# Optimization experiments

Measured on AMD Instinct MI355X. Metric: run time of the kernel, lower is better.

## Reference

```python
import jax, jax.numpy as jnp
import numpy as np

NV, NC, E, D = 100000, 400000, 1600000, 128

def _mlp2(x, w1, b1, w2, b2):
    # Linear->ReLU->Linear->ReLU (weights stored [in, out])
    return jax.nn.relu(jax.nn.relu(x @ w1 + b1) @ w2 + b2)

def setup_inputs() -> dict:
    key = jax.random.key(0)
    ks = jax.random.split(key, 16)
    s = 1.0 / np.sqrt(D)
    return {
        "hv": jax.random.normal(ks[0], (NV, D), jnp.float32),
        "hc": jax.random.normal(ks[1], (NC, D), jnp.float32),
        "row_v": jax.random.randint(ks[2], (E,), 0, NV, jnp.int32),
        "col_v": jax.random.randint(ks[3], (E,), 0, 2 * NC, jnp.int32),
        "row_c": jax.random.randint(ks[4], (E,), 0, NC, jnp.int32),
        "col_c": jax.random.randint(ks[5], (E,), 0, 2 * NV, jnp.int32),
        # message MLPs: order [fmv_pos, fmv_neg, fmc_pos, fmc_neg]
        "mw1": jax.random.normal(ks[6], (4, D, D), jnp.float32) * s,
        "mb1": jax.random.normal(ks[7], (4, D), jnp.float32) * s,
        "mw2": jax.random.normal(ks[8], (4, D, D), jnp.float32) * s,
        "mb2": jax.random.normal(ks[9], (4, D), jnp.float32) * s,
        # update MLPs: order [fuv, fuc]; first layer takes concat(h, m) -> 2D in
        "uw1": jax.random.normal(ks[10], (2, 2 * D, D), jnp.float32) * s,
        "ub1": jax.random.normal(ks[11], (2, D), jnp.float32) * s,
        "uw2": jax.random.normal(ks[12], (2, D, D), jnp.float32) * s,
        "ub2": jax.random.normal(ks[13], (2, D), jnp.float32) * s,
    }

def reference(hv, hc, row_v, col_v, row_c, col_c,
              mw1, mb1, mw2, mb2, uw1, ub1, uw2, ub2):
    nv, nc = hv.shape[0], hc.shape[0]
    # message: transform clause feats with pos/neg MLPs, concat rows, spmm via gather+segment_sum
    zv = jnp.concatenate([
        _mlp2(hc, mw1[0], mb1[0], mw2[0], mb2[0]),  # fmv_pos(hc)
        _mlp2(hc, mw1[1], mb1[1], mw2[1], mb2[1]),  # fmv_neg(hc)
    ], axis=0)                                       # [2*NC, D]
    mv = jax.ops.segment_sum(zv[col_v], row_v, num_segments=nv)  # spmm(vadj, zv)
    zc = jnp.concatenate([
        _mlp2(hv, mw1[2], mb1[2], mw2[2], mb2[2]),  # fmc_pos(hv)
        _mlp2(hv, mw1[3], mb1[3], mw2[3], mb2[3]),  # fmc_neg(hv)
    ], axis=0)                                       # [2*NV, D]
    mc = jax.ops.segment_sum(zc[col_c], row_c, num_segments=nc)  # spmm(cadj, zc)
    # update: concat(h, m) -> MLP
    hv_new = _mlp2(jnp.concatenate([hv, mv], axis=1), uw1[0], ub1[0], uw2[0], ub2[0])
    hc_new = _mlp2(jnp.concatenate([hc, mc], axis=1), uw1[1], ub1[1], uw2[1], ub2[1])
    return (hv_new, hc_new)
```

## Files before the change

kernel.cpp:

```cpp
#include <hip/hip_runtime.h>
#include <hip/hip_bf16.h>

#define NVV 100000
#define NCC 400000
#define NEE 1600000

typedef short short8 __attribute__((ext_vector_type(8)));
typedef short short4v __attribute__((ext_vector_type(4)));
typedef float f32x4 __attribute__((ext_vector_type(4)));
typedef unsigned int u32x2 __attribute__((ext_vector_type(2)));
typedef unsigned int u32x4 __attribute__((ext_vector_type(4)));

__device__ __forceinline__ float b2f(short s) {
    unsigned int u = ((unsigned int)(unsigned short)s) << 16;
    return __builtin_bit_cast(float, u);
}
__device__ __forceinline__ short f2b(float f) {
    __hip_bfloat16 h = __float2bfloat16(f);
    return __builtin_bit_cast(short, h);
}
__device__ __forceinline__ unsigned int cvtpk(float a, float b) {
    unsigned int r;
    asm("v_cvt_pk_bf16_f32 %0, %1, %2" : "=v"(r) : "v"(a), "v"(b));
    return r;
}

__global__ __launch_bounds__(256)
void prep_all(const float* __restrict__ mw1, const float* __restrict__ mw2,
              const float* __restrict__ uw1, const float* __restrict__ uw2,
              short* __restrict__ wt_m1, short* __restrict__ wt_m2,
              short* __restrict__ wt_u1, short* __restrict__ wt_u2)
{
    int e = blockIdx.x * 256 + threadIdx.x;
    const float* W; short* WT; int K; int idx;
    if (e < 65536)        { W = mw1; WT = wt_m1; K = 128; idx = e; }
    else if (e < 131072)  { W = mw2; WT = wt_m2; K = 128; idx = e - 65536; }
    else if (e < 196608)  { W = uw1; WT = wt_u1; K = 256; idx = e - 131072; }
    else if (e < 229376)  { W = uw2; WT = wt_u2; K = 128; idx = e - 196608; }
    else return;
    int mk = idx >> 7, n = idx & 127;
    int mi = mk / K, k = mk - mi * K;
    WT[(size_t)mi * K * 128 + (size_t)n * K + k] = f2b(W[idx]);
}

__global__ __launch_bounds__(256)
void to_bf16_2(const float* __restrict__ hv, const float* __restrict__ hc,
               short* __restrict__ hvb, short* __restrict__ hcb)
{
    const long nv = (long)NVV * 128;
    const long nc = (long)NCC * 128;
    long i0 = ((long)blockIdx.x * 256 + threadIdx.x) * 8;
    long stride = (long)gridDim.x * 256 * 8;
    for (long i = i0; i < nv + nc; i += stride) {
        const float* in; short* outp; long j;
        if (i < nv) { in = hv; outp = hvb; j = i; }
        else        { in = hc; outp = hcb; j = i - nv; }
        f32x4 a = *(const f32x4*)(in + j);
        f32x4 b = *(const f32x4*)(in + j + 4);
        u32x4 o;
        o[0] = cvtpk(a[0], a[1]);
        o[1] = cvtpk(a[2], a[3]);
        o[2] = cvtpk(b[0], b[1]);
        o[3] = cvtpk(b[2], b[3]);
        *(u32x4*)(outp + j) = o;
    }
}

template<int NW>
__global__ __launch_bounds__(NW * 64, 1)
void mlp2_msg_all(const short* __restrict__ hcb, const short* __restrict__ hvb,
                  const short* __restrict__ WT1, const float* __restrict__ B1a,
                  const short* __restrict__ WT2, const float* __restrict__ B2a,
                  short* __restrict__ zv, short* __restrict__ zc, int splitC)
{
    constexpr int BM = NW * 32;
    constexpr int NT = NW * 64;
    __shared__ short sW1[128 * 136];
    __shared__ short sW2[128 * 136];
    __shared__ short sH[BM * 136];

    const int tid = threadIdx.x;
    const int lane = tid & 63;
    const int w = tid >> 6;
    const int p = lane & 15;
    const int q = lane >> 4;

    int b = blockIdx.x;
    const short* X; short* z; int M, c0, cstr, set;
    if (b < splitC) {
        set = b & 1; X = hcb; z = zv + (size_t)set * NCC * 128;
        M = NCC; c0 = b >> 1; cstr = splitC >> 1;
    } else {
        int bb = b - splitC;
        set = 2 + (bb & 1); X = hvb; z = zc + (size_t)(bb & 1) * NVV * 128;
        M = NVV; c0 = bb >> 1; cstr = (gridDim.x - splitC) >> 1;
    }
    const int nChunks = (M + BM - 1) / BM;

    const short* w1g = WT1 + set * 16384;
    const short* w2g = WT2 + set * 16384;
    const float* b1g = B1a + set * 128;
    const float* b2g = B2a + set * 128;

    for (int e = tid * 8; e < 128 * 128; e += NT * 8) {
        int n = e >> 7, k = e & 127;
        *(short8*)(sW1 + n * 136 + k) = *(const short8*)(w1g + e);
        *(short8*)(sW2 + n * 136 + k) = *(const short8*)(w2g + e);
    }
    __syncthreads();

    if (c0 >= nChunks) return;

    short8 xfA[2][4], xfB[2][4];

    auto issueX = [&](short8 (&xf)[2][4], int c) {
        long base = (long)c * BM + w * 32;
        #pragma unroll
        for (int t = 0; t < 2; ++t) {
            long m = base + t * 16 + p;
            if (m > (long)M - 1) m = (long)M - 1;
            const short* src = X + m * 128 + q * 8;
            #pragma unroll
            for (int kk = 0; kk < 4; ++kk)
                xf[t][kk] = *(const short8*)(src + kk * 32);
        }
        __builtin_amdgcn_sched_barrier(0);
    };

    auto computeStore = [&](short8 (&xf)[2][4], int c) {
        long base = (long)c * BM + w * 32;
        f32x4 acc[8][2];
        #pragma unroll
        for (int cc = 0; cc < 8; ++cc)
            #pragma unroll
            for (int t = 0; t < 2; ++t)
                acc[cc][t] = (f32x4){0.f, 0.f, 0.f, 0.f};

        #pragma unroll
        for (int kk = 0; kk < 4; ++kk) {
            short8 af[8];
            #pragma unroll
            for (int cc = 0; cc < 8; ++cc)
                af[cc] = *(const short8*)(sW1 + (cc * 16 + p) * 136 + kk * 32 + q * 8);
            #pragma unroll
            for (int cc = 0; cc < 8; ++cc)
                #pragma unroll
                for (int t = 0; t < 2; ++t)
                    acc[cc][t] = __builtin_amdgcn_mfma_f32_16x16x32_bf16(af[cc], xf[t][kk], acc[cc][t], 0, 0, 0);
        }

        #pragma unroll
        for (int cc = 0; cc < 8; ++cc) {
            f32x4 bb = *(const f32x4*)(b1g + cc * 16 + q * 4);
            #pragma unroll
            for (int t = 0; t < 2; ++t) {
                u32x2 u;
                u[0] = cvtpk(fmaxf(acc[cc][t][0] + bb[0], 0.f), fmaxf(acc[cc][t][1] + bb[1], 0.f));
                u[1] = cvtpk(fmaxf(acc[cc][t][2] + bb[2], 0.f), fmaxf(acc[cc][t][3] + bb[3], 0.f));
                *(u32x2*)(sH + (w * 32 + t * 16 + p) * 136 + cc * 16 + q * 4) = u;
            }
        }
        asm volatile("s_waitcnt lgkmcnt(0)" ::: "memory");

        f32x4 acc2[8][2];
        #pragma unroll
        for (int cc = 0; cc < 8; ++cc)
            #pragma unroll
            for (int t = 0; t < 2; ++t)
                acc2[cc][t] = (f32x4){0.f, 0.f, 0.f, 0.f};

        #pragma unroll
        for (int kk = 0; kk < 4; ++kk) {
            short8 af[8], bfr[2];
            #pragma unroll
            for (int cc = 0; cc < 8; ++cc)
                af[cc] = *(const short8*)(sW2 + (cc * 16 + p) * 136 + kk * 32 + q * 8);
            #pragma unroll
            for (int t = 0; t < 2; ++t)
                bfr[t] = *(const short8*)(sH + (w * 32 + t * 16 + p) * 136 + kk * 32 + q * 8);
            #pragma unroll
            for (int cc = 0; cc < 8; ++cc)
                #pragma unroll
                for (int t = 0; t < 2; ++t)
                    acc2[cc][t] = __builtin_amdgcn_mfma_f32_16x16x32_bf16(af[cc], bfr[t], acc2[cc][t], 0, 0, 0);
        }

        #pragma unroll
        for (int cc = 0; cc < 8; ++cc) {
            f32x4 bb = *(const f32x4*)(b2g + cc * 16 + q * 4);
            #pragma unroll
            for (int t = 0; t < 2; ++t) {
                long m = base + t * 16 + p;
                if (m < M) {
                    u32x2 u;
                    u[0] = cvtpk(fmaxf(acc2[cc][t][0] + bb[0], 0.f), fmaxf(acc2[cc][t][1] + bb[1], 0.f));
                    u[1] = cvtpk(fmaxf(acc2[cc][t][2] + bb[2], 0.f), fmaxf(acc2[cc][t][3] + bb[3], 0.f));
                    *(u32x2*)(z + m * 128 + cc * 16 + q * 4) = u;
                }
            }
        }
    };

    int c = c0;
    issueX(xfA, c);
    while (true) {
        if (c + cstr < nChunks) issueX(xfB, c + cstr);
        computeStore(xfA, c);
        c += cstr; if (c >= nChunks) break;
        if (c + cstr < nChunks) issueX(xfA, c + cstr);
        computeStore(xfB, c);
        c += cstr; if (c >= nChunks) break;
    }
}

template<int NW>
__global__ __launch_bounds__(NW * 64, 1)
void mlp2_upd_all(const short* __restrict__ hvb, const short* __restrict__ hcb,
                  const short* __restrict__ mv, const short* __restrict__ mc,
                  const short* __restrict__ wt_u1, const float* __restrict__ ub1,
                  const short* __restrict__ wt_u2, const float* __restrict__ ub2,
                  float* __restrict__ out, int splitV)
{
    constexpr int BM = NW * 32;
    constexpr int NT = NW * 64;
    __shared__ short sW1[128 * 264];
    __shared__ short sW2[128 * 136];
    __shared__ short sH[BM * 136];

    const int tid = threadIdx.x;
    const int lane = tid & 63;
    const int w = tid >> 6;
    const int p = lane & 15;
    const int q = lane >> 4;

    int b = blockIdx.x;
    const short *X, *X2; float* O; int M, c0, cstr, set;
    if (b < splitV) {
        set = 0; X = hvb; X2 = mv; O = out; M = NVV; c0 = b; cstr = splitV;
    } else {
        set = 1; X = hcb; X2 = mc; O = out + (size_t)NVV * 128; M = NCC;
        c0 = b - splitV; cstr = gridDim.x - splitV;
    }
    const int nChunks = (M + BM - 1) / BM;

    const short* W1T = wt_u1 + set * 32768;
    const short* W2T = wt_u2 + set * 16384;
    const float* B1 = ub1 + set * 128;
    const float* B2 = ub2 + set * 128;

    for (int e = tid * 8; e < 128 * 256; e += NT * 8) {
        int n = e >> 8, k = e & 255;
        *(short8*)(sW1 + n * 264 + k) = *(const short8*)(W1T + e);
    }
    for (int e = tid * 8; e < 128 * 128; e += NT * 8) {
        int n = e >> 7, k = e & 127;
        *(short8*)(sW2 + n * 136 + k) = *(const short8*)(W2T + e);
    }
    __syncthreads();

    if (c0 >= nChunks) return;

    short8 bufA[2][8], bufB[2][8];

    auto issueX = [&](short8 (&xf)[2][8], int c) {
        long base = (long)c * BM + w * 32;
        #pragma unroll
        for (int t = 0; t < 2; ++t) {
            long m = base + t * 16 + p;
            if (m > (long)M - 1) m = (long)M - 1;
            const short* s1 = X + m * 128 + q * 8;
            const short* s2 = X2 + m * 128 + q * 8;
            #pragma unroll
            for (int kk = 0; kk < 4; ++kk) {
                xf[t][kk]     = *(const short8*)(s1 + kk * 32);
                xf[t][kk + 4] = *(const short8*)(s2 + kk * 32);
            }
        }
        __builtin_amdgcn_sched_barrier(0);
    };

    auto computeStore = [&](short8 (&xf)[2][8], int c) {
        long base = (long)c * BM + w * 32;
        f32x4 acc[8][2];
        #pragma unroll
        for (int cc = 0; cc < 8; ++cc)
            #pragma unroll
            for (int t = 0; t < 2; ++t)
                acc[cc][t] = (f32x4){0.f, 0.f, 0.f, 0.f};

        #pragma unroll
        for (int kk = 0; kk < 8; ++kk) {
            short8 af[8];
            #pragma unroll
            for (int cc = 0; cc < 8; ++cc)
                af[cc] = *(const short8*)(sW1 + (cc * 16 + p) * 264 + kk * 32 + q * 8);
            #pragma unroll
            for (int cc = 0; cc < 8; ++cc)
                #pragma unroll
                for (int t = 0; t < 2; ++t)
                    acc[cc][t] = __builtin_amdgcn_mfma_f32_16x16x32_bf16(af[cc], xf[t][kk], acc[cc][t], 0, 0, 0);
        }

        #pragma unroll
        for (int cc = 0; cc < 8; ++cc) {
            f32x4 bb = *(const f32x4*)(B1 + cc * 16 + q * 4);
            #pragma unroll
            for (int t = 0; t < 2; ++t) {
                u32x2 u;
                u[0] = cvtpk(fmaxf(acc[cc][t][0] + bb[0], 0.f), fmaxf(acc[cc][t][1] + bb[1], 0.f));
                u[1] = cvtpk(fmaxf(acc[cc][t][2] + bb[2], 0.f), fmaxf(acc[cc][t][3] + bb[3], 0.f));
                *(u32x2*)(sH + (w * 32 + t * 16 + p) * 136 + cc * 16 + q * 4) = u;
            }
        }
        asm volatile("s_waitcnt lgkmcnt(0)" ::: "memory");

        f32x4 acc2[8][2];
        #pragma unroll
        for (int cc = 0; cc < 8; ++cc)
            #pragma unroll
            for (int t = 0; t < 2; ++t)
                acc2[cc][t] = (f32x4){0.f, 0.f, 0.f, 0.f};

        #pragma unroll
        for (int kk = 0; kk < 4; ++kk) {
            short8 af[8], bfr[2];
            #pragma unroll
            for (int cc = 0; cc < 8; ++cc)
                af[cc] = *(const short8*)(sW2 + (cc * 16 + p) * 136 + kk * 32 + q * 8);
            #pragma unroll
            for (int t = 0; t < 2; ++t)
                bfr[t] = *(const short8*)(sH + (w * 32 + t * 16 + p) * 136 + kk * 32 + q * 8);
            #pragma unroll
            for (int cc = 0; cc < 8; ++cc)
                #pragma unroll
                for (int t = 0; t < 2; ++t)
                    acc2[cc][t] = __builtin_amdgcn_mfma_f32_16x16x32_bf16(af[cc], bfr[t], acc2[cc][t], 0, 0, 0);
        }

        #pragma unroll
        for (int cc = 0; cc < 8; ++cc) {
            f32x4 bb = *(const f32x4*)(B2 + cc * 16 + q * 4);
            #pragma unroll
            for (int t = 0; t < 2; ++t) {
                long m = base + t * 16 + p;
                if (m < M) {
                    f32x4 fv;
                    #pragma unroll
                    for (int i = 0; i < 4; ++i)
                        fv[i] = fmaxf(acc2[cc][t][i] + bb[i], 0.f);
                    *(f32x4*)(O + m * 128 + cc * 16 + q * 4) = fv;
                }
            }
        }
    };

    int c = c0;
    issueX(bufA, c);
    while (true) {
        if (c + cstr < nChunks) issueX(bufB, c + cstr);
        computeStore(bufA, c);
        c += cstr; if (c >= nChunks) break;
        if (c + cstr < nChunks) issueX(bufA, c + cstr);
        computeStore(bufB, c);
        c += cstr; if (c >= nChunks) break;
    }
}


__global__ __launch_bounds__(256)
void hist2(const int* __restrict__ row_v, const int* __restrict__ row_c,
           int* __restrict__ cnt_v, int* __restrict__ cnt_c)
{
    int e = blockIdx.x * 256 + threadIdx.x;
    if (e < NEE) atomicAdd(&cnt_v[row_v[e]], 1);
    else if (e < 2 * NEE) atomicAdd(&cnt_c[row_c[e - NEE]], 1);
}

__global__ __launch_bounds__(256)
void seg_reduce2(const int* __restrict__ cnt_v, const int* __restrict__ cnt_c,
                 int* __restrict__ bsum_v, int* __restrict__ bsum_c, int Bv)
{
    __shared__ int s[256];
    int b = blockIdx.x, t = threadIdx.x;
    const int* counts; int* bsum; int N; int bb;
    if (b < Bv) { counts = cnt_v; bsum = bsum_v; N = NVV; bb = b; }
    else        { counts = cnt_c; bsum = bsum_c; N = NCC; bb = b - Bv; }
    int base = bb * 512;
    int v = 0;
    if (base + t < N) v += counts[base + t];
    if (base + 256 + t < N) v += counts[base + 256 + t];
    s[t] = v;
    __syncthreads();
    for (int off = 128; off > 0; off >>= 1) {
        if (t < off) s[t] += s[t + off];
        __syncthreads();
    }
    if (t == 0) bsum[bb] = s[0];
}

__global__ __launch_bounds__(1024)
void scan_bsum2(int* __restrict__ bsum_v, int* __restrict__ bsum_c, int Bv, int Bc)
{
    __shared__ int s[1024];
    int* bsum = (blockIdx.x == 0) ? bsum_v : bsum_c;
    int B = (blockIdx.x == 0) ? Bv : Bc;
    int t = threadIdx.x;
    s[t] = (t < B) ? bsum[t] : 0;
    __syncthreads();
    for (int off = 1; off < 1024; off <<= 1) {
        int v = (t >= off) ? s[t - off] : 0;
        __syncthreads();
        s[t] += v;
        __syncthreads();
    }
    if (t < B) bsum[t] = (t == 0) ? 0 : s[t - 1];
}

__global__ __launch_bounds__(512)
void scan_final2(const int* __restrict__ cnt_v, const int* __restrict__ cnt_c,
                 const int* __restrict__ bsum_v, const int* __restrict__ bsum_c,
                 int* __restrict__ offs_v, int* __restrict__ offs_c, int Bv)
{
    __shared__ int s[512];
    int b = blockIdx.x, t = threadIdx.x;
    const int* counts; const int* bsum; int* offs; int N; int bb;
    if (b < Bv) { counts = cnt_v; bsum = bsum_v; offs = offs_v; N = NVV; bb = b; }
    else        { counts = cnt_c; bsum = bsum_c; offs = offs_c; N = NCC; bb = b - Bv; }
    int idx = bb * 512 + t;
    int c = (idx < N) ? counts[idx] : 0;
    s[t] = c;
    __syncthreads();
    for (int off = 1; off < 512; off <<= 1) {
        int v = (t >= off) ? s[t - off] : 0;
        __syncthreads();
        s[t] += v;
        __syncthreads();
    }
    if (idx < N) offs[idx] = bsum[bb] + s[t] - c;
    if (idx == N - 1) offs[N] = bsum[bb] + s[t];
}

__global__ __launch_bounds__(256)
void csr_fill2(const int* __restrict__ row_v, const int* __restrict__ col_v,
               const int* __restrict__ row_c, const int* __restrict__ col_c,
               const int* __restrict__ offs_v, const int* __restrict__ offs_c,
               int* __restrict__ cur_v, int* __restrict__ cur_c,
               int* __restrict__ edge_v, int* __restrict__ edge_c)
{
    int e = blockIdx.x * 256 + threadIdx.x;
    if (e < NEE) {
        int r = row_v[e];
        int pos = offs_v[r] + atomicAdd(&cur_v[r], 1);
        edge_v[pos] = col_v[e];
    } else if (e < 2 * NEE) {
        int ee = e - NEE;
        int r = row_c[ee];
        int pos = offs_c[r] + atomicAdd(&cur_c[r], 1);
        edge_c[pos] = col_c[ee];
    }
}

__global__ __launch_bounds__(256)
void csr_gather_all(const short* __restrict__ zv, const short* __restrict__ zc,
                    const int* __restrict__ offs_v, const int* __restrict__ edge_v,
                    const int* __restrict__ offs_c, const int* __restrict__ edge_c,
                    short* __restrict__ mv, short* __restrict__ mc)
{
    int wid = (int)((blockIdx.x * 256 + threadIdx.x) >> 6);
    int lane = threadIdx.x & 63;
    int sub = lane >> 4;
    int sl = lane & 15;
    int row = wid * 4 + sub;
    if (row >= NVV + NCC) return;

    const short* z; const int* offs; const int* ec; short* md; int r;
    if (row < NVV) { z = zv; offs = offs_v; ec = edge_v; md = mv; r = row; }
    else           { z = zc; offs = offs_c; ec = edge_c; md = mc; r = row - NVV; }

    int beg = offs[r], end = offs[r + 1];

    float a[8];
    #pragma unroll
    for (int i = 0; i < 8; ++i) a[i] = 0.f;

    int j = beg;
    for (; j + 3 < end; j += 4) {
        int c0 = ec[j], c1 = ec[j + 1], c2 = ec[j + 2], c3 = ec[j + 3];
        short8 v0 = *(const short8*)(z + (long)c0 * 128 + sl * 8);
        short8 v1 = *(const short8*)(z + (long)c1 * 128 + sl * 8);
        short8 v2 = *(const short8*)(z + (long)c2 * 128 + sl * 8);
        short8 v3 = *(const short8*)(z + (long)c3 * 128 + sl * 8);
        #pragma unroll
        for (int i = 0; i < 8; ++i)
            a[i] += (b2f(v0[i]) + b2f(v1[i])) + (b2f(v2[i]) + b2f(v3[i]));
    }
    for (; j < end; ++j) {
        int c = ec[j];
        short8 v = *(const short8*)(z + (long)c * 128 + sl * 8);
        #pragma unroll
        for (int i = 0; i < 8; ++i) a[i] += b2f(v[i]);
    }

    u32x4 o;
    o[0] = cvtpk(a[0], a[1]);
    o[1] = cvtpk(a[2], a[3]);
    o[2] = cvtpk(a[4], a[5]);
    o[3] = cvtpk(a[6], a[7]);
    *(u32x4*)(md + (long)r * 128 + sl * 8) = o;
}

extern "C" void kernel_launch(void* const* d_in, const int* in_sizes, int n_in,
                              void* d_out, int out_size, void* d_ws, size_t ws_size,
                              hipStream_t stream)
{
    const float* hv   = (const float*)d_in[0];
    const float* hc   = (const float*)d_in[1];
    const int* row_v  = (const int*)d_in[2];
    const int* col_v  = (const int*)d_in[3];
    const int* row_c  = (const int*)d_in[4];
    const int* col_c  = (const int*)d_in[5];
    const float* mw1  = (const float*)d_in[6];
    const float* mb1  = (const float*)d_in[7];
    const float* mw2  = (const float*)d_in[8];
    const float* mb2  = (const float*)d_in[9];
    const float* uw1  = (const float*)d_in[10];
    const float* ub1  = (const float*)d_in[11];
    const float* uw2  = (const float*)d_in[12];
    const float* ub2  = (const float*)d_in[13];
    float* out = (float*)d_out;

    short* zv = (short*)d_ws;
    short* zc = zv + (size_t)2 * NCC * 128;
    short* mv = zc + (size_t)2 * NVV * 128;
    short* mc = mv + (size_t)NVV * 128;
    short* wt_m1 = mc + (size_t)NCC * 128;
    short* wt_m2 = wt_m1 + 4 * 16384;
    short* wt_u1 = wt_m2 + 4 * 16384;
    short* wt_u2 = wt_u1 + 2 * 32768;
    short* hvb = wt_u2 + 2 * 16384;
    short* hcb = hvb + (size_t)NVV * 128;
    int* edge_v = (int*)(hcb + (size_t)NCC * 128);
    int* edge_c = edge_v + NEE;
    int* offs_v = edge_c + NEE;
    int* offs_c = offs_v + (NVV + 1);
    int* cnt_v  = offs_c + (NCC + 1);
    int* cnt_c  = cnt_v + NVV;
    int* bsum_v = cnt_c + NCC;
    int* bsum_c = bsum_v + 1024;

    const int Bv = (NVV + 511) / 512;
    const int Bc = (NCC + 511) / 512;

    prep_all<<<(229376 + 255) / 256, 256, 0, stream>>>(
        mw1, mw2, uw1, uw2, wt_m1, wt_m2, wt_u1, wt_u2);
    to_bf16_2<<<2048, 256, 0, stream>>>(hv, hc, hvb, hcb);

    hipMemsetAsync(cnt_v, 0, (NVV + NCC) * sizeof(int), stream);
    hist2<<<(2 * NEE + 255) / 256, 256, 0, stream>>>(row_v, row_c, cnt_v, cnt_c);
    seg_reduce2<<<Bv + Bc, 256, 0, stream>>>(cnt_v, cnt_c, bsum_v, bsum_c, Bv);
    scan_bsum2<<<2, 1024, 0, stream>>>(bsum_v, bsum_c, Bv, Bc);
    scan_final2<<<Bv + Bc, 512, 0, stream>>>(cnt_v, cnt_c, bsum_v, bsum_c, offs_v, offs_c, Bv);
    hipMemsetAsync(cnt_v, 0, (NVV + NCC) * sizeof(int), stream);
    csr_fill2<<<(2 * NEE + 255) / 256, 256, 0, stream>>>(
        row_v, col_v, row_c, col_c, offs_v, offs_c, cnt_v, cnt_c, edge_v, edge_c);

    mlp2_msg_all<8><<<256, 512, 0, stream>>>(
        hcb, hvb, wt_m1, mb1, wt_m2, mb2, zv, zc, 204);

    csr_gather_all<<<((NVV + NCC) / 4 + 3) / 4, 256, 0, stream>>>(
        zv, zc, offs_v, edge_v, offs_c, edge_c, mv, mc);

    mlp2_upd_all<6><<<256, 384, 0, stream>>>(
        hvb, hcb, mv, mc, wt_u1, ub1, wt_u2, ub2, out, 51);
}
```

Before: 1.187 ms.

## Use inline-asm global loads with explicit vmcnt waits and split update-MLP prefetch

The activation loads in both MLP kernels now go through inline-asm global_load_dwordx4, with hand-placed s_waitcnt vmcnt barriers, so the compiler can no longer insert conservative waits that stall the double-buffered prefetch. In the update kernel the prefetch is split: the h rows for the next chunk are loaded early, and the message rows are loaded into a single buffer after the first GEMM has consumed the current one. This lowers register pressure (three 2x4 buffers instead of two 2x8) while keeping loads overlapped with MFMA work. Hand-managed vmcnt counts are fragile: if the count of outstanding stores or loads differs from what the code assumes, a buffer could be read before its data arrives.

```diff
diff --git a/kernel.cpp b/kernel.cpp
--- a/kernel.cpp
+++ b/kernel.cpp
@@ -24,6 +24,12 @@
     asm("v_cvt_pk_bf16_f32 %0, %1, %2" : "=v"(r) : "v"(a), "v"(b));
     return r;
 }
+__device__ __forceinline__ short8 gload16(const short* p) {
+    short8 d;
+    asm volatile("global_load_dwordx4 %0, %1, off" : "=v"(d) : "v"(p));
+    return d;
+}
+#define SB0() __builtin_amdgcn_sched_barrier(0)
 
 __global__ __launch_bounds__(256)
 void prep_all(const float* __restrict__ mw1, const float* __restrict__ mw2,
@@ -122,12 +128,12 @@
             const short* src = X + m * 128 + q * 8;
             #pragma unroll
             for (int kk = 0; kk < 4; ++kk)
-                xf[t][kk] = *(const short8*)(src + kk * 32);
-        }
-        __builtin_amdgcn_sched_barrier(0);
+                xf[t][kk] = gload16(src + kk * 32);
+        }
+        SB0();
     };
 
-    auto computeStore = [&](short8 (&xf)[2][4], int c) {
+    auto computeStore = [&](const short8 (&xf)[2][4], int c) {
         long base = (long)c * BM + w * 32;
         f32x4 acc[8][2];
         #pragma unroll
@@ -203,13 +209,27 @@
 
     int c = c0;
     issueX(xfA, c);
+    asm volatile("s_waitcnt vmcnt(0)" ::: "memory");
+    SB0();
     while (true) {
-        if (c + cstr < nChunks) issueX(xfB, c + cstr);
-        computeStore(xfA, c);
-        c += cstr; if (c >= nChunks) break;
-        if (c + cstr < nChunks) issueX(xfA, c + cstr);
-        computeStore(xfB, c);
-        c += cstr; if (c >= nChunks) break;
+        {
+            bool hn = (c + cstr < nChunks);
+            if (hn) issueX(xfB, c + cstr);
+            computeStore(xfA, c);
+            c += cstr;
+            if (!hn) return;
+            asm volatile("s_waitcnt vmcnt(16)" ::: "memory");
+            SB0();
+        }
+        {
+            bool hn = (c + cstr < nChunks);
+            if (hn) issueX(xfA, c + cstr);
+            computeStore(xfB, c);
+            c += cstr;
+            if (!hn) return;
+            asm volatile("s_waitcnt vmcnt(16)" ::: "memory");
+            SB0();
+        }
     }
 }
 
@@ -260,26 +280,36 @@
 
     if (c0 >= nChunks) return;
 
-    short8 bufA[2][8], bufB[2][8];
-
-    auto issueX = [&](short8 (&xf)[2][8], int c) {
+    short8 hA[2][4], hB[2][4], mr[2][4];
+
+    auto issueH = [&](short8 (&h)[2][4], int c) {
         long base = (long)c * BM + w * 32;
         #pragma unroll
         for (int t = 0; t < 2; ++t) {
             long m = base + t * 16 + p;
             if (m > (long)M - 1) m = (long)M - 1;
             const short* s1 = X + m * 128 + q * 8;
+            #pragma unroll
+            for (int kk = 0; kk < 4; ++kk)
+                h[t][kk] = gload16(s1 + kk * 32);
+        }
+        SB0();
+    };
+    auto issueM = [&](int c) {
+        long base = (long)c * BM + w * 32;
+        #pragma unroll
+        for (int t = 0; t < 2; ++t) {
+            long m = base + t * 16 + p;
+            if (m > (long)M - 1) m = (long)M - 1;
             const short* s2 = X2 + m * 128 + q * 8;
             #pragma unroll
-            for (int kk = 0; kk < 4; ++kk) {
-                xf[t][kk]     = *(const short8*)(s1 + kk * 32);
-                xf[t][kk + 4] = *(const short8*)(s2 + kk * 32);
-            }
-        }
-        __builtin_amdgcn_sched_barrier(0);
+            for (int kk = 0; kk < 4; ++kk)
+                mr[t][kk] = gload16(s2 + kk * 32);
+        }
+        SB0();
     };
 
-    auto computeStore = [&](short8 (&xf)[2][8], int c) {
+    auto body = [&](const short8 (&h)[2][4], int c, bool hn, int cn) {
         long base = (long)c * BM + w * 32;
         f32x4 acc[8][2];
         #pragma unroll
@@ -297,9 +327,13 @@
             #pragma unroll
             for (int cc = 0; cc < 8; ++cc)
                 #pragma unroll
-                for (int t = 0; t < 2; ++t)
-                    acc[cc][t] = __builtin_amdgcn_mfma_f32_16x16x32_bf16(af[cc], xf[t][kk], acc[cc][t], 0, 0, 0);
-        }
+                for (int t = 0; t < 2; ++t) {
+                    short8 xcur = (kk < 4) ? h[t][kk] : mr[t][kk - 4];
+                    acc[cc][t] = __builtin_amdgcn_mfma_f32_16x16x32_bf16(af[cc], xcur, acc[cc][t], 0, 0, 0);
+                }
+        }
+
+        if (hn) issueM(cn);
 
         #pragma unroll
         for (int cc = 0; cc < 8; ++cc) {
@@ -355,14 +389,29 @@
     };
 
     int c = c0;
-    issueX(bufA, c);
+    issueH(hA, c);
+    issueM(c);
+    asm volatile("s_waitcnt vmcnt(0)" ::: "memory");
+    SB0();
     while (true) {
-        if (c + cstr < nChunks) issueX(bufB, c + cstr);
-        computeStore(bufA, c);
-        c += cstr; if (c >= nChunks) break;
-        if (c + cstr < nChunks) issueX(bufA, c + cstr);
-        computeStore(bufB, c);
-        c += cstr; if (c >= nChunks) break;
+        {
+            bool hn = (c + cstr < nChunks);
+            if (hn) issueH(hB, c + cstr);
+            body(hA, c, hn, c + cstr);
+            c += cstr;
+            if (!hn) return;
+            asm volatile("s_waitcnt vmcnt(16)" ::: "memory");
+            SB0();
+        }
+        {
+            bool hn = (c + cstr < nChunks);
+            if (hn) issueH(hA, c + cstr);
+            body(hB, c, hn, c + cstr);
+            c += cstr;
+            if (!hn) return;
+            asm volatile("s_waitcnt vmcnt(16)" ::: "memory");
+            SB0();
+        }
     }
 }
 
```

After: 1.157 ms. 2.5% less time.
